# Optimization experiments

Hardware: AMD Instinct MI355X
Metric: run time of the kernel (lower is better)

The kernel has to match this reference:

```python
import jax, jax.numpy as jnp
import numpy as np

LEAK = 0.1  # LeakyReLU slope used throughout


def _conv(x, w, b, ph, pw):
    # NCHW conv, stride 1, asymmetric-free padding (ph on H, pw on W)
    y = jax.lax.conv_general_dilated(x, w, (1, 1), ((ph, ph), (pw, pw)),
                                     dimension_numbers=('NCHW', 'OIHW', 'NCHW'))
    return y + b[None, :, None, None]


def _pool2(x):
    B, C, H, W = x.shape
    return x.reshape(B, C, H // 2, 2, W // 2, 2).mean(axis=(3, 5))


def _lrelu(x):
    return jax.nn.leaky_relu(x, LEAK)


def _forward(x, label, g_style, spaced_style, char_style,
             sp1_w, sp2_w, in_w, in_b, c1w1, c1b1, c1w2, c1b2, c2w, c2b,
             c3w1, c3b1, c3w2, c3b2, fm_w, fm_b,
             cd_conv_w, cd_conv_b, cd_fc1_w, cd_fc1_b, cd_fc2_w, cd_fc2_b):
    B = x.shape[0]
    style1 = g_style @ sp1_w.T              # [B, dim//2]
    style2 = g_style @ sp2_w.T              # [B, dim]
    h = _lrelu(_conv(x, in_w, in_b, 0, 3))  # [B,dim,58,W]
    h = jnp.concatenate([h, jnp.broadcast_to(style1[:, :, None, None],
                        (B, style1.shape[1], h.shape[2], h.shape[3]))], axis=1)
    h = _lrelu(_conv(h, c1w1, c1b1, 0, 1))
    h = _pool2(h)
    m = _lrelu(_conv(h, c1w2, c1b2, 0, 1))  # [B,2dim,26,W/2]
    m2 = jnp.concatenate([m, jnp.broadcast_to(style2[:, :, None, None],
                         (B, style2.shape[1], m.shape[2], m.shape[3]))], axis=1)
    mL = _pool2(_lrelu(_conv(m2, c2w, c2b, 0, 1)))  # [B,2dim,12,W/4]
    lab = jnp.transpose(label, (1, 2, 0))           # [B, n_class, T]
    cls = jnp.argmax(lab, axis=1)                   # [B, T]
    hL, wL = mL.shape[2], mL.shape[3]
    lab_e = jnp.broadcast_to(lab[:, :, None, :], (B, lab.shape[1], hL, lab.shape[2]))
    sc = jnp.transpose(spaced_style, (1, 2, 0))     # [B, char_style_size, T]
    sc_e = jnp.broadcast_to(sc[:, :, None, :], (B, sc.shape[1], hL, sc.shape[2]))
    sal = jnp.concatenate([sc_e, lab_e], axis=1)[:, :, :, :wL]  # T == wL -> diff = 0
    mL = jnp.concatenate([mL, sal], axis=1)
    mL = _lrelu(_conv(mL, c3w1, c3b1, 0, 1))
    mL = _pool2(mL)
    mL = _lrelu(_conv(mL, c3w2, c3b2, 0, 1))        # [B, 4dim, 3, W/8]
    pM = _conv(mL, fm_w, fm_b, 0, 1)                # [B, 1, 1, W/8]
    # ---- per-character window gather + per-class expert dispatch ----
    T = label.shape[0]
    win = 2                                          # self.window
    mLp = jnp.pad(mL, ((0, 0), (0, 0), (0, 0), (win, win)))
    idx = jnp.arange(T) // 2                         # i = (i_orig + 0)//2 since diff==0
    cols = idx[:, None] + jnp.arange(2 * win + 1)    # [T,5] window cols in padded coords
    p = mLp[:, :, :, cols]                           # [B, 4dim, 3, T, 5]
    C4 = p.shape[1]
    p = jnp.transpose(p, (0, 3, 1, 2, 4)).reshape(B * T, C4, 3, 5)
    # CharDisc conv: 3x3 valid on [3,5] -> output 1x3; unfold the 3 windows
    wins = jnp.stack([p[..., w:w + 3] for w in range(3)], axis=1)  # [N,3,C4,3,3]
    pw = wins.reshape(B * T, 3, -1)                  # [N, 3, C4*9]
    cls_f = cls.reshape(-1)                          # [N] (all > 0 by construction)
    b_idx = jnp.repeat(jnp.arange(B), T)
    E = cd_conv_w.shape[0]
    Wsel = cd_conv_w.reshape(E, cd_conv_w.shape[1], -1)[cls_f]     # [N, 2dim, C4*9]
    co = jnp.einsum('nwd,nod->nwo', pw, Wsel) + cd_conv_b[cls_f][:, None, :]
    pooled = _lrelu(co).mean(axis=1)                 # conv -> LeakyReLU -> adaptive avg pool
    feat = jnp.concatenate([pooled, char_style[b_idx, cls_f]], axis=-1)  # [N, 2dim+cs]
    h1 = jax.nn.relu(jnp.einsum('nd,ndo->no', feat, cd_fc1_w[cls_f]) + cd_fc1_b[cls_f])
    pChar = jnp.einsum('nd,ndo->no', h1, cd_fc2_w[cls_f]) + cd_fc2_b[cls_f]  # [N,1]
    return pM, pChar


def setup_inputs():
    key = jax.random.key(0)
    ks = jax.random.split(key, 32)
    B, T, H, W = 2, 128, 64, 512
    NC, SS, CS, dim = 80, 256, 32, 64
    s = 0.05
    def rn(i, shape):
        return jax.random.normal(ks[i], shape, jnp.float32) * s
    cls_ids = jax.random.randint(ks[0], (T, B), 1, NC)  # class 0 = blank, never emitted
    return dict(
        x=jax.random.normal(ks[1], (B, 1, H, W), jnp.float32),
        label=jax.nn.one_hot(cls_ids, NC, dtype=jnp.float32),
        g_style=jax.random.normal(ks[2], (B, SS), jnp.float32),
        spaced_style=jax.random.normal(ks[3], (T, B, CS), jnp.float32),
        char_style=jax.random.normal(ks[4], (B, NC, CS), jnp.float32),
        sp1_w=rn(5, (dim // 2, SS)),
        sp2_w=rn(6, (dim, SS)),
        in_w=rn(7, (dim, 1, 7, 7)), in_b=rn(8, (dim,)),
        c1w1=rn(9, (dim, dim // 2 + dim, 3, 3)), c1b1=rn(10, (dim,)),
        c1w2=rn(11, (2 * dim, dim, 3, 3)), c1b2=rn(12, (2 * dim,)),
        c2w=rn(13, (2 * dim, dim + 2 * dim, 3, 3)), c2b=rn(14, (2 * dim,)),
        c3w1=rn(15, (2 * dim, NC + CS + 2 * dim, 3, 3)), c3b1=rn(16, (2 * dim,)),
        c3w2=rn(17, (4 * dim, 2 * dim, 3, 3)), c3b2=rn(18, (4 * dim,)),
        fm_w=rn(19, (1, 4 * dim, 3, 3)), fm_b=rn(20, (1,)),
        cd_conv_w=rn(21, (NC, 2 * dim, 4 * dim, 3, 3)), cd_conv_b=rn(22, (NC, 2 * dim)),
        cd_fc1_w=rn(23, (NC, 2 * dim + CS, 2 * dim)), cd_fc1_b=rn(24, (NC, 2 * dim)),
        cd_fc2_w=rn(25, (NC, 2 * dim, 1)), cd_fc2_b=rn(26, (NC, 1)),
    )


def reference(x, label, g_style, spaced_style, char_style,
              sp1_w, sp2_w, in_w, in_b, c1w1, c1b1, c1w2, c1b2, c2w, c2b,
              c3w1, c3b1, c3w2, c3b2, fm_w, fm_b,
              cd_conv_w, cd_conv_b, cd_fc1_w, cd_fc1_b, cd_fc2_w, cd_fc2_b):
    return _forward(x, label, g_style, spaced_style, char_style,
                    sp1_w, sp2_w, in_w, in_b, c1w1, c1b1, c1w2, c1b2, c2w, c2b,
                    c3w1, c3b1, c3w2, c3b2, fm_w, fm_b,
                    cd_conv_w, cd_conv_b, cd_fc1_w, cd_fc1_b, cd_fc2_w, cd_fc2_b)
```

## Files before the change

### kernel.cpp

```cpp
#include <hip/hip_runtime.h>
#include <hip/hip_bf16.h>

#define LEAKC 0.1f

__device__ __forceinline__ float lrelu(float v){ return v > 0.f ? v : LEAKC*v; }
__device__ __forceinline__ ushort f2b(float f){
  __hip_bfloat16 h = __float2bfloat16(f);
  return *reinterpret_cast<ushort*>(&h);
}
__device__ __forceinline__ float b2f(ushort u){
  __hip_bfloat16 h = *reinterpret_cast<__hip_bfloat16*>(&u);
  return __bfloat162float(h);
}

typedef __attribute__((ext_vector_type(8))) short bf16x8;
typedef __attribute__((ext_vector_type(4))) float f32x4;

__device__ __forceinline__ void pack1(int idx, const float* __restrict__ w,
                                      ushort* __restrict__ wb, int CM, int CTOT){
  int c = idx % CM; int r = idx / CM; int t = r % 9; int n = r / 9;
  wb[idx] = f2b(w[((size_t)n*CTOT + c)*9 + t]);
}

__global__ __launch_bounds__(256) void prep_kernel(
    const float* __restrict__ g, const float* __restrict__ sp1, const float* __restrict__ sp2,
    const float* __restrict__ c1w1, const float* __restrict__ c1b1,
    const float* __restrict__ c1w2,
    const float* __restrict__ c2w,  const float* __restrict__ c2b,
    const float* __restrict__ c3w1, const float* __restrict__ c3b1,
    const float* __restrict__ c3w2,
    const float* __restrict__ label, const float* __restrict__ spaced,
    float* __restrict__ map1, float* __restrict__ map2, float* __restrict__ map6,
    int* __restrict__ clsb, int* __restrict__ cnt, int* __restrict__ off, int* __restrict__ order,
    ushort* __restrict__ Wb2, ushort* __restrict__ Wb4, ushort* __restrict__ Wb5,
    ushort* __restrict__ Wb6, ushort* __restrict__ Wb7){
  int t = threadIdx.x;
  int bid = blockIdx.x;
  if (bid == 0){
    __shared__ float s1s[64], s2s[128];
    if (t < 64){
      int b = t >> 5, j = t & 31;
      float a = 0.f;
      for (int k=0;k<256;k++) a += g[b*256+k]*sp1[j*256+k];
      s1s[t] = a;
    } else if (t < 192){
      int u = t - 64;
      int b = u >> 6, j = u & 63;
      float a = 0.f;
      for (int k=0;k<256;k++) a += g[b*256+k]*sp2[j*256+k];
      s2s[u] = a;
    }
    __syncthreads();
    if (t < 128){
      int b = t >> 6, o = t & 63;
      float S0=0.f,S1=0.f,S2=0.f;
      for (int c=0;c<32;c++){
        float s = s1s[b*32+c];
        const float* wq = c1w1 + ((size_t)o*96 + 64 + c)*9;
        S0 += s*(wq[0]+wq[3]+wq[6]);
        S1 += s*(wq[1]+wq[4]+wq[7]);
        S2 += s*(wq[2]+wq[5]+wq[8]);
      }
      float bb = c1b1[o];
      map1[t*3+0]=S1+S2+bb; map1[t*3+1]=S0+S1+S2+bb; map1[t*3+2]=S0+S1+bb;
    }
    {
      int b = t >> 7, o = t & 127;
      float S0=0.f,S1=0.f,S2=0.f;
      for (int c=0;c<64;c++){
        float s = s2s[b*64+c];
        const float* wq = c2w + ((size_t)o*192 + 128 + c)*9;
        S0 += s*(wq[0]+wq[3]+wq[6]);
        S1 += s*(wq[1]+wq[4]+wq[7]);
        S2 += s*(wq[2]+wq[5]+wq[8]);
      }
      float bb = c2b[o];
      map2[t*3+0]=S1+S2+bb; map2[t*3+1]=S0+S1+S2+bb; map2[t*3+2]=S0+S1+bb;
    }
  } else if (bid == 1){
    __shared__ int h[80], hoff[80];
    if (t < 80) h[t] = 0;
    __syncthreads();
    int b = t >> 7, tt = t & 127;
    const float* p = label + (tt*2 + b)*80;
    float best = p[0]; int bi = 0;
    for (int c=1;c<80;c++){ float v = p[c]; if (v > best){ best = v; bi = c; } }
    clsb[t] = bi;
    atomicAdd(&h[bi], 1);
    __syncthreads();
    if (t == 0){
      int s = 0;
      for (int e=0;e<80;e++){ hoff[e] = s; s += h[e]; }
    }
    __syncthreads();
    if (t < 80){ cnt[t] = h[t]; off[t] = hoff[t]; }
    __syncthreads();
    int rank = atomicAdd(&hoff[bi], 1);
    order[rank] = t;
  } else if (bid < 130){
    int n = (bid - 2)*256 + t;
    int w = n & 127, o = (n >> 7) & 127, b = n >> 14;
    float a = c3b1[o];
    #pragma unroll
    for (int tt=0;tt<3;tt++){
      int j = w + tt - 1;
      if (j < 0 || j >= 128) continue;
      const float* sp = spaced + (j*2 + b)*32;
      const float* lb = label + (j*2 + b)*80;
      for (int c=0;c<32;c++){
        const float* wq = c3w1 + ((size_t)o*240 + 128 + c)*9 + tt;
        a += sp[c]*(wq[0]+wq[3]+wq[6]);
      }
      for (int c=0;c<80;c++){
        const float* wq = c3w1 + ((size_t)o*240 + 160 + c)*9 + tt;
        a += lb[c]*(wq[0]+wq[3]+wq[6]);
      }
    }
    map6[n] = a;
  } else {
    int i = (bid - 130)*256 + t;
    if      (i < 36864)  pack1(i,        c1w1, Wb2, 64, 96);
    else if (i < 110592) pack1(i-36864,  c1w2, Wb4, 64, 64);
    else if (i < 258048) pack1(i-110592, c2w,  Wb5, 128, 192);
    else if (i < 405504) pack1(i-258048, c3w1, Wb6, 128, 240);
    else if (i < 700416) pack1(i-405504, c3w2, Wb7, 128, 128);
  }
}

__global__ void conv_in_kernel(const float* __restrict__ x,
                               const float* __restrict__ wgt,
                               const float* __restrict__ bias,
                               ushort* __restrict__ out){
  int hw = blockIdx.x*256 + threadIdx.x;
  int y = hw >> 9, w = hw & 511;
  int b = blockIdx.z;
  int o0 = blockIdx.y * 8;
  float acc[8];
  #pragma unroll
  for (int i=0;i<8;i++) acc[i] = bias[o0+i];
  for (int kh=0;kh<7;kh++){
    const float* ip = x + (b*64 + y + kh)*512;
    #pragma unroll
    for (int kw=0;kw<7;kw++){
      int wi = w + kw - 3;
      float v = (wi>=0 && wi<512) ? ip[wi] : 0.f;
      #pragma unroll
      for (int i=0;i<8;i++) acc[i] += v * wgt[(o0+i)*49 + kh*7 + kw];
    }
  }
  #pragma unroll
  for (int i=0;i<8;i++)
    out[((b*64 + o0+i)*58 + y)*512 + w] = f2b(lrelu(acc[i]));
}

template<int CM,int WID,int HIN,int COUT,int MODE,int OUTBF>
__global__ __launch_bounds__(256) void conv_mfma(
    const ushort* __restrict__ in,
    const ushort* __restrict__ Wb,
    const float*  __restrict__ mb,
    float* __restrict__ outf,
    ushort* __restrict__ outh){
  constexpr int HOUT = HIN - 2;
  constexpr int KTOT = CM*9;
  constexpr int SLABS = CM/32;
  constexpr int NST = 3*SLABS;
  __shared__ ushort A[2][66][40];
  int tid = threadIdx.x, lane = tid & 63, wave = tid >> 6;
  int mt = blockIdx.x;
  int y  = mt / (WID/64), w0 = (mt % (WID/64))*64;
  int n0 = blockIdx.y*64;
  int b  = blockIdx.z;

  f32x4 acc[4];
  #pragma unroll
  for (int nf=0;nf<4;nf++) acc[nf] = (f32x4){0.f,0.f,0.f,0.f};

  auto stage = [&](int s, int bufi){
    int kh = s / SLABS;
    int c0 = (s % SLABS)*32;
    const ushort* base = in + ((size_t)(b*CM + c0)*HIN + (y+kh))*WID;
    int c2 = (tid & 15)*2, m0v = (tid >> 4)*2*2;
    const ushort* p0 = base + (size_t)c2*HIN*WID + w0 + m0v;
    const ushort* p1 = p0 + (size_t)HIN*WID;
    ushort4 va = *(const ushort4*)p0;
    ushort4 vb = *(const ushort4*)p1;
    uint* dst = (uint*)&A[bufi][1+m0v][c2];
    dst[0]  = (uint)va.x | ((uint)vb.x << 16);
    dst[20] = (uint)va.y | ((uint)vb.y << 16);
    dst[40] = (uint)va.z | ((uint)vb.z << 16);
    dst[60] = (uint)va.w | ((uint)vb.w << 16);
    if (tid < 64){
      int c = tid & 31, side = tid >> 5;
      int w = side ? (w0 + 64) : (w0 - 1);
      ushort v = 0;
      if (w >= 0 && w < WID) v = base[(size_t)c*HIN*WID + w];
      A[bufi][side ? 65 : 0][c] = v;
    }
  };

  stage(0, 0);
  __syncthreads();
  for (int s = 0; s < NST; ++s){
    int cur = s & 1;
    if (s + 1 < NST) stage(s+1, cur ^ 1);
    int kh = s / SLABS;
    int c0 = (s % SLABS)*32;
    #pragma unroll
    for (int kw = 0; kw < 3; ++kw){
      bf16x8 a = *(bf16x8*)&A[cur][wave*16 + (lane & 15) + kw][(lane >> 4)*8];
      #pragma unroll
      for (int nf = 0; nf < 4; ++nf){
        const ushort* wp = Wb + (size_t)(n0 + nf*16 + (lane & 15))*KTOT
                              + (kh*3 + kw)*CM + c0 + (lane >> 4)*8;
        bf16x8 bb = *(const bf16x8*)wp;
        acc[nf] = __builtin_amdgcn_mfma_f32_16x16x32_bf16(a, bb, acc[nf], 0, 0, 0);
      }
    }
    __syncthreads();
  }

  int mrow = wave*16 + ((lane >> 4) << 2);
  int w = w0 + mrow;
  #pragma unroll
  for (int nf = 0; nf < 4; ++nf){
    int n = n0 + nf*16 + (lane & 15);
    float r0 = acc[nf][0], r1 = acc[nf][1], r2 = acc[nf][2], r3 = acc[nf][3];
    if (MODE == 0){
      float bb = mb[n];
      r0 += bb; r1 += bb; r2 += bb; r3 += bb;
    } else if (MODE == 1){
      const float* m3 = mb + (size_t)(b*COUT + n)*3;
      float mL = m3[0], mM = m3[1], mR = m3[2];
      r0 += (w == 0) ? mL : ((w   == WID-1) ? mR : mM);
      r1 += (w+1 == WID-1) ? mR : mM;
      r2 += (w+2 == WID-1) ? mR : mM;
      r3 += (w+3 == WID-1) ? mR : mM;
    } else {
      const float* m6 = mb + ((size_t)(b*COUT + n))*WID + w;
      r0 += m6[0]; r1 += m6[1]; r2 += m6[2]; r3 += m6[3];
    }
    r0 = lrelu(r0); r1 = lrelu(r1); r2 = lrelu(r2); r3 = lrelu(r3);
    size_t off = ((size_t)(b*COUT + n)*HOUT + y)*WID + w;
    if (OUTBF){
      ushort4 o = make_ushort4(f2b(r0), f2b(r1), f2b(r2), f2b(r3));
      *(ushort4*)(outh + off) = o;
    } else {
      *(float4*)(outf + off) = make_float4(r0, r1, r2, r3);
    }
  }
}

__global__ void pool2_h2h_kernel(const ushort* __restrict__ in, ushort* __restrict__ out,
                                 int H, int W, int total){
  int n = blockIdx.x*256 + threadIdx.x;
  if (n >= total) return;
  int Wo = W >> 1;
  int wo = n % Wo;
  int r = n / Wo;
  int Ho = H >> 1;
  int ho = r % Ho;
  int bc = r / Ho;
  const ushort* p = in + (bc*H + 2*ho)*W + 2*wo;
  out[n] = f2b(0.25f*(b2f(p[0]) + b2f(p[1]) + b2f(p[W]) + b2f(p[W+1])));
}

__global__ __launch_bounds__(256) void fmim_kernel(const float* __restrict__ A7,
                          const float* __restrict__ fw,
                          const float* __restrict__ fb,
                          float* __restrict__ out,
                          ushort* __restrict__ pwgh){
  if (blockIdx.x < 128){
    __shared__ float red[4];
    int n = blockIdx.x;
    int b = n >> 6, w = n & 63;
    int c = threadIdx.x;
    float a = 0.f;
    #pragma unroll
    for (int r=0;r<3;r++){
      const float* ip = A7 + ((b*256+c)*3+r)*64;
      const float* wp = fw + (c*3+r)*3;
      #pragma unroll
      for (int kw=0;kw<3;kw++){
        int wi = w + kw - 1;
        if (wi>=0 && wi<64) a += ip[wi]*wp[kw];
      }
    }
    #pragma unroll
    for (int off=32; off>0; off>>=1) a += __shfl_down(a, off, 64);
    if ((threadIdx.x & 63) == 0) red[threadIdx.x>>6] = a;
    __syncthreads();
    if (threadIdx.x == 0) out[n] = red[0]+red[1]+red[2]+red[3] + fb[0];
  } else {
    int i = (blockIdx.x - 128)*256 + threadIdx.x;
    if (i >= 256*3*2304) return;
    int d = i % 2304; int rj = i / 2304; int j = rj % 3; int n = rj / 3;
    int b = n >> 7, t = n & 127; int idx = t >> 1;
    int c = d / 9, rem = d - c*9, r = rem / 3, kw = rem - r*3;
    int col = idx - 2 + kw + j;
    pwgh[i] = (col >= 0 && col < 64) ? f2b(A7[((size_t)(b*256 + c)*3 + r)*64 + col]) : (ushort)0;
  }
}

__global__ __launch_bounds__(256) void cd_conv_kernel(
    const ushort* __restrict__ pwgh,
    const int*   __restrict__ cnt,
    const int*   __restrict__ offv,
    const int*   __restrict__ order,
    const float* __restrict__ Wc,
    float* __restrict__ comat)
{
  __shared__ int rowOff[48];
  __shared__ f32x4 red[4][3][64];
  int e = blockIdx.x, og = blockIdx.y;
  int m = cnt[e];
  if (m == 0) return;
  int base = offv[e];
  int tid = threadIdx.x, lane = tid & 63, wave = tid >> 6;

  const float* wb_base = Wc + ((size_t)(e*128) + og*16 + (lane & 15))*2304;
  int kbase = wave*576 + ((lane >> 4)*8);

  for (int s0 = 0; s0 < m; s0 += 16){
    int rowsChunk = 3*(m - s0); if (rowsChunk > 48) rowsChunk = 48;
    if (tid < 48){
      int lr = s0 + tid/3;
      rowOff[tid] = (lr < m) ? (order[base+lr]*3 + (tid - (tid/3)*3))*2304 : -1;
    }
    __syncthreads();

    int offA[3];
    #pragma unroll
    for (int mt=0; mt<3; mt++) offA[mt] = rowOff[mt*16 + (lane & 15)];

    f32x4 acc[3];
    #pragma unroll
    for (int mt=0; mt<3; mt++) acc[mt] = (f32x4){0.f,0.f,0.f,0.f};

    for (int kk = 0; kk < 18; ++kk){
      int k0 = kbase + kk*32;
      const float* wb = wb_base + k0;
      float4 wv0 = *(const float4*)wb;
      float4 wv1 = *(const float4*)(wb + 4);
      bf16x8 bfr = { (short)f2b(wv0.x), (short)f2b(wv0.y), (short)f2b(wv0.z), (short)f2b(wv0.w),
                     (short)f2b(wv1.x), (short)f2b(wv1.y), (short)f2b(wv1.z), (short)f2b(wv1.w) };
      #pragma unroll
      for (int mt=0; mt<3; mt++){
        if (mt*16 < rowsChunk){
          bf16x8 af = {0,0,0,0,0,0,0,0};
          if (offA[mt] >= 0) af = *(const bf16x8*)&pwgh[offA[mt] + k0];
          acc[mt] = __builtin_amdgcn_mfma_f32_16x16x32_bf16(af, bfr, acc[mt], 0, 0, 0);
        }
      }
    }

    #pragma unroll
    for (int mt=0; mt<3; mt++) red[wave][mt][lane] = acc[mt];
    __syncthreads();

    if (wave < 3){
      int mt = wave;
      if (mt*16 < rowsChunk){
        f32x4 s4 = red[0][mt][lane];
        #pragma unroll
        for (int w2=1; w2<4; w2++){
          f32x4 t4 = red[w2][mt][lane];
          s4[0]+=t4[0]; s4[1]+=t4[1]; s4[2]+=t4[2]; s4[3]+=t4[3];
        }
        int col = og*16 + (lane & 15);
        #pragma unroll
        for (int r=0; r<4; r++){
          int row = mt*16 + ((lane >> 4) << 2) + r;
          if (row < rowsChunk){
            int lrank = s0 + row/3, j = row - (row/3)*3;
            int n = order[base + lrank];
            comat[((size_t)n*128 + col)*3 + j] = s4[r];
          }
        }
      }
    }
    __syncthreads();
  }
}

__global__ __launch_bounds__(128) void cd_tail_kernel(
    const float* __restrict__ comat,
    const int*   __restrict__ clsb,
    const float* __restrict__ bcv,
    const float* __restrict__ cstyle,
    const float* __restrict__ W1,
    const float* __restrict__ b1,
    const float* __restrict__ W2,
    const float* __restrict__ b2,
    float* __restrict__ pChar)
{
  __shared__ float feat[160];
  __shared__ float red2[2];
  int n = blockIdx.x, tid = threadIdx.x;
  int b = n >> 7;
  int e = clsb[n];
  int o = tid;
  const float* cm = comat + ((size_t)n*128 + o)*3;
  float bb = bcv[e*128 + o];
  feat[o] = (lrelu(cm[0]+bb) + lrelu(cm[1]+bb) + lrelu(cm[2]+bb)) * (1.f/3.f);
  if (tid < 32) feat[128+tid] = cstyle[(b*80 + e)*32 + tid];
  __syncthreads();

  float s = b1[e*128 + o];
  for (int d=0;d<160;d++) s += feat[d]*W1[(e*160 + d)*128 + o];
  float h = s > 0.f ? s : 0.f;
  float contrib = h * W2[e*128 + o];
  #pragma unroll
  for (int off=32; off>0; off>>=1) contrib += __shfl_down(contrib, off, 64);
  if ((tid & 63) == 0) red2[tid>>6] = contrib;
  __syncthreads();
  if (tid == 0) pChar[n] = red2[0] + red2[1] + b2[e];
}

extern "C" void kernel_launch(void* const* d_in, const int* in_sizes, int n_in,
                              void* d_out, int out_size, void* d_ws, size_t ws_size,
                              hipStream_t stream){
  (void)in_sizes; (void)n_in; (void)out_size; (void)ws_size;
  const float* x      = (const float*)d_in[0];
  const float* label  = (const float*)d_in[1];
  const float* g_style= (const float*)d_in[2];
  const float* spaced = (const float*)d_in[3];
  const float* cstyle = (const float*)d_in[4];
  const float* sp1    = (const float*)d_in[5];
  const float* sp2    = (const float*)d_in[6];
  const float* in_w   = (const float*)d_in[7];
  const float* in_b   = (const float*)d_in[8];
  const float* c1w1   = (const float*)d_in[9];
  const float* c1b1   = (const float*)d_in[10];
  const float* c1w2   = (const float*)d_in[11];
  const float* c1b2   = (const float*)d_in[12];
  const float* c2w    = (const float*)d_in[13];
  const float* c2b    = (const float*)d_in[14];
  const float* c3w1   = (const float*)d_in[15];
  const float* c3b1   = (const float*)d_in[16];
  const float* c3w2   = (const float*)d_in[17];
  const float* c3b2   = (const float*)d_in[18];
  const float* fm_w   = (const float*)d_in[19];
  const float* fm_b   = (const float*)d_in[20];
  const float* cdw    = (const float*)d_in[21];
  const float* cdb    = (const float*)d_in[22];
  const float* fc1w   = (const float*)d_in[23];
  const float* fc1b   = (const float*)d_in[24];
  const float* fc2w   = (const float*)d_in[25];
  const float* fc2b   = (const float*)d_in[26];
  float* out = (float*)d_out;
  char* ws = (char*)d_ws;

  ushort* h1b  = (ushort*)(ws + 0);
  ushort* A2h  = (ushort*)(ws + 7602176);
  ushort* pwgh = (ushort*)(ws + 7602176);
  ushort* P3b  = (ushort*)(ws + 22282240);
  ushort* A4b  = (ushort*)(ws + 24117248);
  ushort* A5h  = (ushort*)(ws + 27525120);
  ushort* P5b  = (ushort*)(ws + 33816576);
  ushort* A6b  = (ushort*)(ws + 34603008);
  ushort* P6b  = (ushort*)(ws + 35258368);
  float*  A7   = (float*) (ws + 35422208);
  float*  comat= (float*) (ws + 36995072);
  ushort* Wb2  = (ushort*)(ws + 37388288);
  ushort* Wb4  = (ushort*)(ws + 37462016);
  ushort* Wb5  = (ushort*)(ws + 37609472);
  ushort* Wb6  = (ushort*)(ws + 37904384);
  ushort* Wb7  = (ushort*)(ws + 38199296);
  float*  map6 = (float*) (ws + 38789120);
  float*  map1 = (float*) (ws + 38920192);
  float*  map2 = (float*) (ws + 38921728);
  int*    clsb = (int*)   (ws + 38924800);
  int*    order= (int*)   (ws + 38925824);
  int*    cntv = (int*)   (ws + 38926848);
  int*    offv = (int*)   (ws + 38927168);

  prep_kernel<<<2866,256,0,stream>>>(g_style, sp1, sp2, c1w1, c1b1, c1w2, c2w, c2b,
                                     c3w1, c3b1, c3w2, label, spaced,
                                     map1, map2, map6, clsb, cntv, offv, order,
                                     Wb2, Wb4, Wb5, Wb6, Wb7);

  conv_in_kernel<<<dim3(116,8,2),256,0,stream>>>(x, in_w, in_b, h1b);
  conv_mfma<64,512,58,64,1,1><<<dim3(448,1,2),256,0,stream>>>(h1b, Wb2, map1, nullptr, A2h);
  pool2_h2h_kernel<<<3584,256,0,stream>>>(A2h, P3b, 56, 512, 917504);
  conv_mfma<64,256,28,128,0,1><<<dim3(104,2,2),256,0,stream>>>(P3b, Wb4, c1b2, nullptr, A4b);
  conv_mfma<128,256,26,128,1,1><<<dim3(96,2,2),256,0,stream>>>(A4b, Wb5, map2, nullptr, A5h);
  pool2_h2h_kernel<<<1536,256,0,stream>>>(A5h, P5b, 24, 256, 393216);
  conv_mfma<128,128,12,128,2,1><<<dim3(20,2,2),256,0,stream>>>(P5b, Wb6, map6, nullptr, A6b);
  pool2_h2h_kernel<<<320,256,0,stream>>>(A6b, P6b, 10, 128, 81920);
  conv_mfma<128,64,5,256,0,0><<<dim3(3,4,2),256,0,stream>>>(P6b, Wb7, c3b2, A7, nullptr);
  fmim_kernel<<<7040,256,0,stream>>>(A7, fm_w, fm_b, out, pwgh);
  cd_conv_kernel<<<dim3(80,8),256,0,stream>>>(pwgh, cntv, offv, order, cdw, comat);
  cd_tail_kernel<<<256,128,0,stream>>>(comat, clsb, cdb, cstyle, fc1w, fc1b, fc2w, fc2b, out + 128);
}
```

Before: 282.0 us.

## Fuse 2x2 avg-pool into conv staging and merge input conv into prep

The three standalone pool2 kernels are removed. Each following conv_mfma now computes the 2x2 average directly while staging its input tile into shared memory, reading the unpooled bf16 activations. The 7x7 input convolution is moved into the prep kernel as extra blocks, so it runs alongside the weight packing instead of in its own launch. This cuts kernel launches and the pooled intermediate round-trips through memory. The cost is that each conv stage reads four times as many input elements and recomputes the pooled values for every kh/slab stage.

```diff
diff --git a/kernel.cpp b/kernel.cpp
--- a/kernel.cpp
+++ b/kernel.cpp
@@ -15,6 +15,7 @@
 
 typedef __attribute__((ext_vector_type(8))) short bf16x8;
 typedef __attribute__((ext_vector_type(4))) float f32x4;
+typedef __attribute__((ext_vector_type(8))) unsigned short ushort8;
 
 __device__ __forceinline__ void pack1(int idx, const float* __restrict__ w,
                                       ushort* __restrict__ wb, int CM, int CTOT){
@@ -30,10 +31,12 @@
     const float* __restrict__ c3w1, const float* __restrict__ c3b1,
     const float* __restrict__ c3w2,
     const float* __restrict__ label, const float* __restrict__ spaced,
+    const float* __restrict__ x, const float* __restrict__ in_w, const float* __restrict__ in_b,
     float* __restrict__ map1, float* __restrict__ map2, float* __restrict__ map6,
     int* __restrict__ clsb, int* __restrict__ cnt, int* __restrict__ off, int* __restrict__ order,
     ushort* __restrict__ Wb2, ushort* __restrict__ Wb4, ushort* __restrict__ Wb5,
-    ushort* __restrict__ Wb6, ushort* __restrict__ Wb7){
+    ushort* __restrict__ Wb6, ushort* __restrict__ Wb7,
+    ushort* __restrict__ h1b){
   int t = threadIdx.x;
   int bid = blockIdx.x;
   if (bid == 0){
@@ -117,43 +120,41 @@
       }
     }
     map6[n] = a;
-  } else {
+  } else if (bid < 2866){
     int i = (bid - 130)*256 + t;
     if      (i < 36864)  pack1(i,        c1w1, Wb2, 64, 96);
     else if (i < 110592) pack1(i-36864,  c1w2, Wb4, 64, 64);
     else if (i < 258048) pack1(i-110592, c2w,  Wb5, 128, 192);
     else if (i < 405504) pack1(i-258048, c3w1, Wb6, 128, 240);
     else if (i < 700416) pack1(i-405504, c3w2, Wb7, 128, 128);
+  } else {
+    int bid2 = bid - 2866;
+    int xb = bid2 % 116;
+    int og = (bid2 / 116) & 7;
+    int b  = bid2 / (116*8);
+    int hw = xb*256 + t;
+    int y = hw >> 9, w = hw & 511;
+    int o0 = og * 8;
+    float acc[8];
+    #pragma unroll
+    for (int i=0;i<8;i++) acc[i] = in_b[o0+i];
+    for (int kh=0;kh<7;kh++){
+      const float* ip = x + ((size_t)b*64 + y + kh)*512;
+      #pragma unroll
+      for (int kw=0;kw<7;kw++){
+        int wi = w + kw - 3;
+        float v = (wi>=0 && wi<512) ? ip[wi] : 0.f;
+        #pragma unroll
+        for (int i=0;i<8;i++) acc[i] += v * in_w[(o0+i)*49 + kh*7 + kw];
+      }
+    }
+    #pragma unroll
+    for (int i=0;i<8;i++)
+      h1b[((size_t)(b*64 + o0+i)*58 + y)*512 + w] = f2b(lrelu(acc[i]));
   }
 }
 
-__global__ void conv_in_kernel(const float* __restrict__ x,
-                               const float* __restrict__ wgt,
-                               const float* __restrict__ bias,
-                               ushort* __restrict__ out){
-  int hw = blockIdx.x*256 + threadIdx.x;
-  int y = hw >> 9, w = hw & 511;
-  int b = blockIdx.z;
-  int o0 = blockIdx.y * 8;
-  float acc[8];
-  #pragma unroll
-  for (int i=0;i<8;i++) acc[i] = bias[o0+i];
-  for (int kh=0;kh<7;kh++){
-    const float* ip = x + (b*64 + y + kh)*512;
-    #pragma unroll
-    for (int kw=0;kw<7;kw++){
-      int wi = w + kw - 3;
-      float v = (wi>=0 && wi<512) ? ip[wi] : 0.f;
-      #pragma unroll
-      for (int i=0;i<8;i++) acc[i] += v * wgt[(o0+i)*49 + kh*7 + kw];
-    }
-  }
-  #pragma unroll
-  for (int i=0;i<8;i++)
-    out[((b*64 + o0+i)*58 + y)*512 + w] = f2b(lrelu(acc[i]));
-}
-
-template<int CM,int WID,int HIN,int COUT,int MODE,int OUTBF>
+template<int CM,int WID,int HIN,int COUT,int MODE,int OUTBF,int POOLIN>
 __global__ __launch_bounds__(256) void conv_mfma(
     const ushort* __restrict__ in,
     const ushort* __restrict__ Wb,
@@ -164,6 +165,8 @@
   constexpr int KTOT = CM*9;
   constexpr int SLABS = CM/32;
   constexpr int NST = 3*SLABS;
+  constexpr int HINF = 2*HIN;
+  constexpr int WIDF = 2*WID;
   __shared__ ushort A[2][66][40];
   int tid = threadIdx.x, lane = tid & 63, wave = tid >> 6;
   int mt = blockIdx.x;
@@ -177,24 +180,49 @@
 
   auto stage = [&](int s, int bufi){
     int kh = s / SLABS;
-    int c0 = (s % SLABS)*32;
-    const ushort* base = in + ((size_t)(b*CM + c0)*HIN + (y+kh))*WID;
-    int c2 = (tid & 15)*2, m0v = (tid >> 4)*2*2;
-    const ushort* p0 = base + (size_t)c2*HIN*WID + w0 + m0v;
-    const ushort* p1 = p0 + (size_t)HIN*WID;
-    ushort4 va = *(const ushort4*)p0;
-    ushort4 vb = *(const ushort4*)p1;
+    int c0s = (s % SLABS)*32;
+    int c2 = (tid & 15)*2, m0v = (tid >> 4)*4;
     uint* dst = (uint*)&A[bufi][1+m0v][c2];
-    dst[0]  = (uint)va.x | ((uint)vb.x << 16);
-    dst[20] = (uint)va.y | ((uint)vb.y << 16);
-    dst[40] = (uint)va.z | ((uint)vb.z << 16);
-    dst[60] = (uint)va.w | ((uint)vb.w << 16);
-    if (tid < 64){
-      int c = tid & 31, side = tid >> 5;
-      int w = side ? (w0 + 64) : (w0 - 1);
-      ushort v = 0;
-      if (w >= 0 && w < WID) v = base[(size_t)c*HIN*WID + w];
-      A[bufi][side ? 65 : 0][c] = v;
+    if (POOLIN){
+      const ushort* q0 = in + ((size_t)(b*CM + c0s + c2)*HINF + 2*(y+kh))*WIDF + 2*(w0 + m0v);
+      const ushort* q1 = q0 + (size_t)HINF*WIDF;
+      ushort8 a0 = *(const ushort8*)q0;
+      ushort8 a1 = *(const ushort8*)(q0 + WIDF);
+      ushort8 b0 = *(const ushort8*)q1;
+      ushort8 b1 = *(const ushort8*)(q1 + WIDF);
+      #pragma unroll
+      for (int k=0;k<4;k++){
+        float pa = 0.25f*(b2f(a0[2*k])+b2f(a0[2*k+1])+b2f(a1[2*k])+b2f(a1[2*k+1]));
+        float pb = 0.25f*(b2f(b0[2*k])+b2f(b0[2*k+1])+b2f(b1[2*k])+b2f(b1[2*k+1]));
+        dst[k*20] = (uint)f2b(pa) | ((uint)f2b(pb) << 16);
+      }
+      if (tid < 64){
+        int c = tid & 31, side = tid >> 5;
+        int wp = side ? (w0 + 64) : (w0 - 1);
+        ushort v = 0;
+        if (wp >= 0 && wp < WID){
+          const ushort* q = in + ((size_t)(b*CM + c0s + c)*HINF + 2*(y+kh))*WIDF + 2*wp;
+          v = f2b(0.25f*(b2f(q[0])+b2f(q[1])+b2f(q[WIDF])+b2f(q[WIDF+1])));
+        }
+        A[bufi][side ? 65 : 0][c] = v;
+      }
+    } else {
+      const ushort* base = in + ((size_t)(b*CM + c0s)*HIN + (y+kh))*WID;
+      const ushort* p0 = base + (size_t)c2*HIN*WID + w0 + m0v;
+      const ushort* p1 = p0 + (size_t)HIN*WID;
+      ushort4 va = *(const ushort4*)p0;
+      ushort4 vb = *(const ushort4*)p1;
+      dst[0]  = (uint)va.x | ((uint)vb.x << 16);
+      dst[20] = (uint)va.y | ((uint)vb.y << 16);
+      dst[40] = (uint)va.z | ((uint)vb.z << 16);
+      dst[60] = (uint)va.w | ((uint)vb.w << 16);
+      if (tid < 64){
+        int c = tid & 31, side = tid >> 5;
+        int w = side ? (w0 + 64) : (w0 - 1);
+        ushort v = 0;
+        if (w >= 0 && w < WID) v = base[(size_t)c*HIN*WID + w];
+        A[bufi][side ? 65 : 0][c] = v;
+      }
     }
   };
 
@@ -248,20 +276,6 @@
       *(float4*)(outf + off) = make_float4(r0, r1, r2, r3);
     }
   }
-}
-
-__global__ void pool2_h2h_kernel(const ushort* __restrict__ in, ushort* __restrict__ out,
-                                 int H, int W, int total){
-  int n = blockIdx.x*256 + threadIdx.x;
-  if (n >= total) return;
-  int Wo = W >> 1;
-  int wo = n % Wo;
-  int r = n / Wo;
-  int Ho = H >> 1;
-  int ho = r % Ho;
-  int bc = r / Ho;
-  const ushort* p = in + (bc*H + 2*ho)*W + 2*wo;
-  out[n] = f2b(0.25f*(b2f(p[0]) + b2f(p[1]) + b2f(p[W]) + b2f(p[W+1])));
 }
 
 __global__ __launch_bounds__(256) void fmim_kernel(const float* __restrict__ A7,
@@ -452,42 +466,36 @@
 
   ushort* h1b  = (ushort*)(ws + 0);
   ushort* A2h  = (ushort*)(ws + 7602176);
-  ushort* pwgh = (ushort*)(ws + 7602176);
-  ushort* P3b  = (ushort*)(ws + 22282240);
-  ushort* A4b  = (ushort*)(ws + 24117248);
-  ushort* A5h  = (ushort*)(ws + 27525120);
-  ushort* P5b  = (ushort*)(ws + 33816576);
-  ushort* A6b  = (ushort*)(ws + 34603008);
-  ushort* P6b  = (ushort*)(ws + 35258368);
-  float*  A7   = (float*) (ws + 35422208);
-  float*  comat= (float*) (ws + 36995072);
-  ushort* Wb2  = (ushort*)(ws + 37388288);
-  ushort* Wb4  = (ushort*)(ws + 37462016);
-  ushort* Wb5  = (ushort*)(ws + 37609472);
-  ushort* Wb6  = (ushort*)(ws + 37904384);
-  ushort* Wb7  = (ushort*)(ws + 38199296);
-  float*  map6 = (float*) (ws + 38789120);
-  float*  map1 = (float*) (ws + 38920192);
-  float*  map2 = (float*) (ws + 38921728);
-  int*    clsb = (int*)   (ws + 38924800);
-  int*    order= (int*)   (ws + 38925824);
-  int*    cntv = (int*)   (ws + 38926848);
-  int*    offv = (int*)   (ws + 38927168);
-
-  prep_kernel<<<2866,256,0,stream>>>(g_style, sp1, sp2, c1w1, c1b1, c1w2, c2w, c2b,
+  ushort* pwgh = (ushort*)(ws + 14942208);
+  ushort* A4b  = (ushort*)(ws + 18481152);
+  ushort* A5h  = (ushort*)(ws + 21889024);
+  ushort* A6b  = (ushort*)(ws + 25034752);
+  float*  A7   = (float*) (ws + 25690112);
+  float*  comat= (float*) (ws + 27262976);
+  ushort* Wb2  = (ushort*)(ws + 27656192);
+  ushort* Wb4  = (ushort*)(ws + 27729920);
+  ushort* Wb5  = (ushort*)(ws + 27877376);
+  ushort* Wb6  = (ushort*)(ws + 28172288);
+  ushort* Wb7  = (ushort*)(ws + 28467200);
+  float*  map6 = (float*) (ws + 29057024);
+  float*  map1 = (float*) (ws + 29188096);
+  float*  map2 = (float*) (ws + 29189632);
+  int*    clsb = (int*)   (ws + 29192704);
+  int*    order= (int*)   (ws + 29193728);
+  int*    cntv = (int*)   (ws + 29194752);
+  int*    offv = (int*)   (ws + 29195072);
+
+  prep_kernel<<<4722,256,0,stream>>>(g_style, sp1, sp2, c1w1, c1b1, c1w2, c2w, c2b,
                                      c3w1, c3b1, c3w2, label, spaced,
+                                     x, in_w, in_b,
                                      map1, map2, map6, clsb, cntv, offv, order,
-                                     Wb2, Wb4, Wb5, Wb6, Wb7);
-
-  conv_in_kernel<<<dim3(116,8,2),256,0,stream>>>(x, in_w, in_b, h1b);
-  conv_mfma<64,512,58,64,1,1><<<dim3(448,1,2),256,0,stream>>>(h1b, Wb2, map1, nullptr, A2h);
-  pool2_h2h_kernel<<<3584,256,0,stream>>>(A2h, P3b, 56, 512, 917504);
-  conv_mfma<64,256,28,128,0,1><<<dim3(104,2,2),256,0,stream>>>(P3b, Wb4, c1b2, nullptr, A4b);
-  conv_mfma<128,256,26,128,1,1><<<dim3(96,2,2),256,0,stream>>>(A4b, Wb5, map2, nullptr, A5h);
-  pool2_h2h_kernel<<<1536,256,0,stream>>>(A5h, P5b, 24, 256, 393216);
-  conv_mfma<128,128,12,128,2,1><<<dim3(20,2,2),256,0,stream>>>(P5b, Wb6, map6, nullptr, A6b);
-  pool2_h2h_kernel<<<320,256,0,stream>>>(A6b, P6b, 10, 128, 81920);
-  conv_mfma<128,64,5,256,0,0><<<dim3(3,4,2),256,0,stream>>>(P6b, Wb7, c3b2, A7, nullptr);
+                                     Wb2, Wb4, Wb5, Wb6, Wb7, h1b);
+
+  conv_mfma<64,512,58,64,1,1,0><<<dim3(448,1,2),256,0,stream>>>(h1b, Wb2, map1, nullptr, A2h);
+  conv_mfma<64,256,28,128,0,1,1><<<dim3(104,2,2),256,0,stream>>>(A2h, Wb4, c1b2, nullptr, A4b);
+  conv_mfma<128,256,26,128,1,1,0><<<dim3(96,2,2),256,0,stream>>>(A4b, Wb5, map2, nullptr, A5h);
+  conv_mfma<128,128,12,128,2,1,1><<<dim3(20,2,2),256,0,stream>>>(A5h, Wb6, map6, nullptr, A6b);
+  conv_mfma<128,64,5,256,0,0,1><<<dim3(3,4,2),256,0,stream>>>(A6b, Wb7, c3b2, A7, nullptr);
   fmim_kernel<<<7040,256,0,stream>>>(A7, fm_w, fm_b, out, pwgh);
   cd_conv_kernel<<<dim3(80,8),256,0,stream>>>(pwgh, cntv, offv, order, cdw, comat);
   cd_tail_kernel<<<256,128,0,stream>>>(comat, clsb, cdb, cstyle, fc1w, fc1b, fc2w, fc2b, out + 128);
```

Result: faster. 249.4 us, median of 3 (-11.6%).
